# Optimization experiments

Hardware: AMD Instinct MI355X
Metric: run time of the kernel (lower is better)

The kernel has to match this reference:

```python
import jax, jax.numpy as jnp
import numpy as np

D_MODEL = 1040
N_HEADS = 16
FEAT = 32            # feature_dim
HEAD_DIM = 65        # d_model // num_heads; must equal 2*FEAT+1 for the z-division to broadcast
EPS = 1e-9


def setup_inputs() -> dict:
    key = jax.random.key(0)
    k1, k2, k3, k4, k5, k6 = jax.random.split(key, 6)
    B, S = 4, 4096
    scale = 1.0 / np.sqrt(D_MODEL)
    return {
        "hidden_states": jax.random.normal(k1, (B, S, D_MODEL), dtype=jnp.float32),
        "attention_mask": jax.random.randint(k2, (B, S), 0, 2, dtype=jnp.int32),
        "Wq": jax.random.normal(k3, (D_MODEL, N_HEADS * FEAT), dtype=jnp.float32) * scale,
        "Wk": jax.random.normal(k4, (D_MODEL, N_HEADS * FEAT), dtype=jnp.float32) * scale,
        "Wv": jax.random.normal(k5, (D_MODEL, N_HEADS * HEAD_DIM), dtype=jnp.float32) * scale,
        "Wo": jax.random.normal(k6, (N_HEADS * HEAD_DIM, D_MODEL), dtype=jnp.float32) * scale,
    }


def _phi(x):
    # polynomial feature map: [1, x, 0.5*x^2] -> last dim 2*FEAT+1
    return jnp.concatenate([jnp.ones_like(x[..., :1]), x, 0.5 * x * x], axis=-1)


def reference(hidden_states, attention_mask, Wq, Wk, Wv, Wo):
    B, S, _ = hidden_states.shape
    # projections -> [B, H, S, d]
    q = (hidden_states @ Wq).reshape(B, S, N_HEADS, FEAT).transpose(0, 2, 1, 3)
    k = (hidden_states @ Wk).reshape(B, S, N_HEADS, FEAT).transpose(0, 2, 1, 3)
    v = (hidden_states @ Wv).reshape(B, S, N_HEADS, HEAD_DIM).transpose(0, 2, 1, 3)
    q = _phi(q)  # [B, H, S, D] with D = 2*FEAT+1
    k = _phi(k)
    # linear attention: KV state then query it
    kv = jnp.einsum('bhnd,bhne->bhde', k, v)        # [B, H, D, HEAD_DIM]
    qkv = jnp.einsum('bhnd,bhde->bhne', q, kv)      # [B, H, S, HEAD_DIM]
    # z = einsum('bhnd,bhne->bhne', q, k.sum(n, keepdim)) with size-1 broadcast on n:
    # contracts d of q against k.sum's d-slot, i.e. (sum_d q) outer (sum_n k)
    z = jnp.sum(q, axis=-1, keepdims=True) * jnp.sum(k, axis=2, keepdims=True)  # [B,H,S,D]
    out = qkv / (z + EPS)                            # requires HEAD_DIM == D
    out = jnp.where(attention_mask[:, None, :, None] == 0, 0.0, out)
    out = out.transpose(0, 2, 1, 3).reshape(B, S, N_HEADS * HEAD_DIM)
    return out @ Wo
```

## Files before the change

kernel.cpp:

```cpp
#include <hip/hip_runtime.h>
#include <hip/hip_bf16.h>

typedef unsigned short ushort_t;
typedef unsigned int uint_t;

#define S_LEN 4096
#define BATCH 4
#define DMODEL 1040
#define KPAD 1056
#define KO 1152
#define NPADW 1152
#define M_H 8192
#define KVSPLIT 32

using f32x4 = __attribute__((ext_vector_type(4))) float;
using bf16x8 = __attribute__((ext_vector_type(8))) __bf16;
using f16x8 = __attribute__((ext_vector_type(8))) _Float16;

__device__ __forceinline__ void splitf16(float x, ushort_t& h, ushort_t& l) {
  _Float16 hf = (_Float16)x;
  float r = (x - (float)hf) * 4096.0f;
  _Float16 lf = (_Float16)r;
  h = __builtin_bit_cast(ushort_t, hf);
  l = __builtin_bit_cast(ushort_t, lf);
}

typedef const __attribute__((address_space(1))) unsigned int* gas_u32p;
typedef __attribute__((address_space(3))) unsigned int* las_u32p;
__device__ __forceinline__ void gload_lds16(const ushort_t* g, ushort_t* l) {
  __builtin_amdgcn_global_load_lds((gas_u32p)g, (las_u32p)l, 16, 0, 0);
}

__device__ __forceinline__ void tile_map(int lid, int NT, int& m0, int& n0) {
  const int x = lid & 7, pos = lid >> 3;
  const int mi = pos / NT, ni = pos - mi * NT;
  m0 = (x * 8 + mi) * 128;
  n0 = ni * 128;
}

union pack8 { ushort_t u[8]; uint4 v; };

__global__ __launch_bounds__(256) void split_hs_kernel(const float* __restrict__ hs,
                                                       ushort_t* __restrict__ hh,
                                                       ushort_t* __restrict__ hl) {
  const int C8 = KPAD / 8;
  int idx = blockIdx.x * 256 + threadIdx.x;
  if (idx >= M_H * C8) return;
  int row = idx / C8, col = (idx % C8) * 8;
  pack8 ph, pl;
  if (col < DMODEL) {
    const float* p = &hs[(size_t)row * DMODEL + col];
#pragma unroll
    for (int j = 0; j < 8; ++j) splitf16(p[j], ph.u[j], pl.u[j]);
  } else {
#pragma unroll
    for (int j = 0; j < 8; ++j) { ph.u[j] = 0; pl.u[j] = 0; }
  }
  size_t o = (size_t)row * KPAD + col;
  *reinterpret_cast<uint4*>(&hh[o]) = ph.v;
  *reinterpret_cast<uint4*>(&hl[o]) = pl.v;
}

__global__ __launch_bounds__(256) void split_wqk_kernel(const float* __restrict__ Wq,
                                                        const float* __restrict__ Wk,
                                                        ushort_t* __restrict__ th,
                                                        ushort_t* __restrict__ tl) {
  const int C8 = KPAD / 8;
  int idx = blockIdx.x * 256 + threadIdx.x;
  if (idx >= 1024 * C8) return;
  int n = idx / C8, k = (idx % C8) * 8;
  pack8 ph, pl;
#pragma unroll
  for (int j = 0; j < 8; ++j) {
    int kk = k + j;
    float val = 0.f;
    if (kk < DMODEL) val = (n < 512) ? Wq[(size_t)kk * 512 + n] : Wk[(size_t)kk * 512 + (n - 512)];
    splitf16(val, ph.u[j], pl.u[j]);
  }
  size_t o = (size_t)n * KPAD + k;
  *reinterpret_cast<uint4*>(&th[o]) = ph.v;
  *reinterpret_cast<uint4*>(&tl[o]) = pl.v;
}

__global__ __launch_bounds__(256) void split_wv_kernel(const float* __restrict__ Wv,
                                                       ushort_t* __restrict__ th) {
  const int C8 = KPAD / 8;
  int idx = blockIdx.x * 256 + threadIdx.x;
  if (idx >= NPADW * C8) return;
  int n = idx / C8, k = (idx % C8) * 8;
  pack8 ph;
#pragma unroll
  for (int j = 0; j < 8; ++j) {
    int kk = k + j;
    float val = (n < DMODEL && kk < DMODEL) ? Wv[(size_t)kk * DMODEL + n] : 0.f;
    ph.u[j] = __builtin_bit_cast(ushort_t, (_Float16)val);
  }
  *reinterpret_cast<uint4*>(&th[(size_t)n * KPAD + k]) = ph.v;
}

__global__ __launch_bounds__(256) void split_wo_kernel(const float* __restrict__ Wo,
                                                       ushort_t* __restrict__ th) {
  const int C8O = KO / 8;
  int idx = blockIdx.x * 256 + threadIdx.x;
  if (idx >= NPADW * C8O) return;
  int n = idx / C8O, k = (idx % C8O) * 8;
  pack8 ph;
#pragma unroll
  for (int j = 0; j < 8; ++j) {
    int kk = k + j;
    int h = kk / 72, e = kk % 72;
    float val = (n < DMODEL && e < 65) ? Wo[(size_t)(h * 65 + e) * DMODEL + n] : 0.f;
    ph.u[j] = __builtin_bit_cast(ushort_t, __float2bfloat16(val));
  }
  *reinterpret_cast<uint4*>(&th[(size_t)n * KO + k]) = ph.v;
}

__global__ __launch_bounds__(512, 4) void gemm_qk(const ushort_t* __restrict__ Ahg,
                                                  const ushort_t* __restrict__ Alg,
                                                  const ushort_t* __restrict__ Bhg,
                                                  const ushort_t* __restrict__ Blg,
                                                  float* __restrict__ C, int kdim) {
  __shared__ ushort_t Ah[2][4096], Al[2][4096], Bh[2][4096], Bl[2][4096];
  const int t = threadIdx.x;
  const int w = t >> 6, l = t & 63;
  int m0, n0;
  tile_map(blockIdx.x, 8, m0, n0);
  const int wm = w >> 2, wn = w & 3;
  const int row16 = l & 15, g = l >> 4;

  f32x4 acc[4][2], acc2[4][2];
#pragma unroll
  for (int m = 0; m < 4; ++m)
#pragma unroll
    for (int n = 0; n < 2; ++n) { acc[m][n] = (f32x4){0,0,0,0}; acc2[m][n] = (f32x4){0,0,0,0}; }

  const int chunk = t;
  const int r0 = chunk >> 2;
  const int ch0 = (chunk & 3) ^ ((r0 ^ (r0 >> 2)) & 3);

#define STAGE_QK(K0, BUF)                                                       \
  {                                                                             \
    const size_t ga = (size_t)(m0 + r0) * kdim + (K0) + ch0 * 8;                \
    const size_t gb = (size_t)(n0 + r0) * kdim + (K0) + ch0 * 8;                \
    gload_lds16(Ahg + ga, &Ah[BUF][chunk * 8]);                                 \
    gload_lds16(Alg + ga, &Al[BUF][chunk * 8]);                                 \
    gload_lds16(Bhg + gb, &Bh[BUF][chunk * 8]);                                 \
    gload_lds16(Blg + gb, &Bl[BUF][chunk * 8]);                                 \
  }

  STAGE_QK(0, 0);
  __syncthreads();
  for (int k0 = 0, it = 0; k0 < kdim; k0 += 32, ++it) {
    const int cur = it & 1;
    if (k0 + 32 < kdim) STAGE_QK(k0 + 32, cur ^ 1);
    f16x8 fah[4], fal[4], fbh[2], fbl[2];
#pragma unroll
    for (int f = 0; f < 4; ++f) {
      const int ra = wm * 64 + f * 16 + row16;
      const int ca = (g ^ ((ra ^ (ra >> 2)) & 3)) << 3;
      fah[f] = *(const f16x8*)&Ah[cur][ra * 32 + ca];
      fal[f] = *(const f16x8*)&Al[cur][ra * 32 + ca];
    }
#pragma unroll
    for (int f = 0; f < 2; ++f) {
      const int rb = wn * 32 + f * 16 + row16;
      const int cb = (g ^ ((rb ^ (rb >> 2)) & 3)) << 3;
      fbh[f] = *(const f16x8*)&Bh[cur][rb * 32 + cb];
      fbl[f] = *(const f16x8*)&Bl[cur][rb * 32 + cb];
    }
#pragma unroll
    for (int m = 0; m < 4; ++m)
#pragma unroll
      for (int n = 0; n < 2; ++n) {
        acc[m][n]  = __builtin_amdgcn_mfma_f32_16x16x32_f16(fah[m], fbh[n], acc[m][n], 0, 0, 0);
        acc2[m][n] = __builtin_amdgcn_mfma_f32_16x16x32_f16(fah[m], fbl[n], acc2[m][n], 0, 0, 0);
        acc2[m][n] = __builtin_amdgcn_mfma_f32_16x16x32_f16(fal[m], fbh[n], acc2[m][n], 0, 0, 0);
      }
    __syncthreads();
  }
#undef STAGE_QK

  const float S2 = 1.0f / 4096.0f;
#pragma unroll
  for (int m = 0; m < 4; ++m)
#pragma unroll
    for (int n = 0; n < 2; ++n) {
      const int col = n0 + wn * 32 + n * 16 + row16;
      const int rowb = m0 + wm * 64 + m * 16 + g * 4;
#pragma unroll
      for (int i = 0; i < 4; ++i)
        C[(size_t)(rowb + i) * 1024 + col] = acc[m][n][i] + acc2[m][n][i] * S2;
    }
}

__global__ __launch_bounds__(256, 4) void gemm_v(const ushort_t* __restrict__ Ahg,
                                                 const ushort_t* __restrict__ Bhg,
                                                 ushort_t* __restrict__ Cv, int kdim) {
  __shared__ ushort_t Ah[2][4096], Bh[2][4096];
  const int t = threadIdx.x;
  const int w = t >> 6, l = t & 63;
  int m0, n0;
  tile_map(blockIdx.x, 9, m0, n0);
  const int wm = w >> 1, wn = w & 1;
  const int row16 = l & 15, g = l >> 4;

  f32x4 acc[4][4];
#pragma unroll
  for (int m = 0; m < 4; ++m)
#pragma unroll
    for (int n = 0; n < 4; ++n) acc[m][n] = (f32x4){0,0,0,0};

  const int chunk0 = (w * 2 + 0) * 64 + l;
  const int chunk1 = (w * 2 + 1) * 64 + l;
  const int r0 = chunk0 >> 2, r1 = chunk1 >> 2;
  const int ch0 = (chunk0 & 3) ^ ((r0 ^ (r0 >> 2)) & 3);
  const int ch1 = (chunk1 & 3) ^ ((r1 ^ (r1 >> 2)) & 3);

#define STAGE_V(K0, BUF)                                                        \
  {                                                                             \
    const size_t ga0 = (size_t)(m0 + r0) * kdim + (K0) + ch0 * 8;               \
    const size_t gb0 = (size_t)(n0 + r0) * kdim + (K0) + ch0 * 8;               \
    const size_t ga1 = (size_t)(m0 + r1) * kdim + (K0) + ch1 * 8;               \
    const size_t gb1 = (size_t)(n0 + r1) * kdim + (K0) + ch1 * 8;               \
    gload_lds16(Ahg + ga0, &Ah[BUF][chunk0 * 8]);                               \
    gload_lds16(Bhg + gb0, &Bh[BUF][chunk0 * 8]);                               \
    gload_lds16(Ahg + ga1, &Ah[BUF][chunk1 * 8]);                               \
    gload_lds16(Bhg + gb1, &Bh[BUF][chunk1 * 8]);                               \
  }

  STAGE_V(0, 0);
  __syncthreads();
  for (int k0 = 0, it = 0; k0 < kdim; k0 += 32, ++it) {
    const int cur = it & 1;
    if (k0 + 32 < kdim) STAGE_V(k0 + 32, cur ^ 1);
    f16x8 fah[4], fbh[4];
#pragma unroll
    for (int f = 0; f < 4; ++f) {
      const int ra = wm * 64 + f * 16 + row16;
      const int ca = (g ^ ((ra ^ (ra >> 2)) & 3)) << 3;
      fah[f] = *(const f16x8*)&Ah[cur][ra * 32 + ca];
      const int rb = wn * 64 + f * 16 + row16;
      const int cb = (g ^ ((rb ^ (rb >> 2)) & 3)) << 3;
      fbh[f] = *(const f16x8*)&Bh[cur][rb * 32 + cb];
    }
#pragma unroll
    for (int m = 0; m < 4; ++m)
#pragma unroll
      for (int n = 0; n < 4; ++n)
        acc[m][n] = __builtin_amdgcn_mfma_f32_16x16x32_f16(fah[m], fbh[n], acc[m][n], 0, 0, 0);
    __syncthreads();
  }
#undef STAGE_V

#pragma unroll
  for (int m = 0; m < 4; ++m)
#pragma unroll
    for (int n = 0; n < 4; ++n) {
      const int col = n0 + wn * 64 + n * 16 + row16;
      const int rowb = m0 + wm * 64 + m * 16 + g * 4;
#pragma unroll
      for (int i = 0; i < 4; ++i)
        Cv[(size_t)(rowb + i) * 1152 + col] =
            __builtin_bit_cast(ushort_t, (_Float16)acc[m][n][i]);
    }
}

__global__ __launch_bounds__(256, 4) void gemm_o(const ushort_t* __restrict__ Ahg,
                                                 const ushort_t* __restrict__ Bhg,
                                                 float* __restrict__ C, int kdim) {
  __shared__ ushort_t Ah[2][4096], Bh[2][4096];
  const int t = threadIdx.x;
  const int w = t >> 6, l = t & 63;
  int m0, n0;
  tile_map(blockIdx.x, 9, m0, n0);
  const int wm = w >> 1, wn = w & 1;
  const int row16 = l & 15, g = l >> 4;

  f32x4 acc[4][4];
#pragma unroll
  for (int m = 0; m < 4; ++m)
#pragma unroll
    for (int n = 0; n < 4; ++n) acc[m][n] = (f32x4){0,0,0,0};

  const int chunk0 = (w * 2 + 0) * 64 + l;
  const int chunk1 = (w * 2 + 1) * 64 + l;
  const int r0 = chunk0 >> 2, r1 = chunk1 >> 2;
  const int ch0 = (chunk0 & 3) ^ ((r0 ^ (r0 >> 2)) & 3);
  const int ch1 = (chunk1 & 3) ^ ((r1 ^ (r1 >> 2)) & 3);

#define STAGE_O(K0, BUF)                                                        \
  {                                                                             \
    const size_t ga0 = (size_t)(m0 + r0) * kdim + (K0) + ch0 * 8;               \
    const size_t gb0 = (size_t)(n0 + r0) * kdim + (K0) + ch0 * 8;               \
    const size_t ga1 = (size_t)(m0 + r1) * kdim + (K0) + ch1 * 8;               \
    const size_t gb1 = (size_t)(n0 + r1) * kdim + (K0) + ch1 * 8;               \
    gload_lds16(Ahg + ga0, &Ah[BUF][chunk0 * 8]);                               \
    gload_lds16(Bhg + gb0, &Bh[BUF][chunk0 * 8]);                               \
    gload_lds16(Ahg + ga1, &Ah[BUF][chunk1 * 8]);                               \
    gload_lds16(Bhg + gb1, &Bh[BUF][chunk1 * 8]);                               \
  }

  STAGE_O(0, 0);
  __syncthreads();
  for (int k0 = 0, it = 0; k0 < kdim; k0 += 32, ++it) {
    const int cur = it & 1;
    if (k0 + 32 < kdim) STAGE_O(k0 + 32, cur ^ 1);
    bf16x8 fah[4], fbh[4];
#pragma unroll
    for (int f = 0; f < 4; ++f) {
      const int ra = wm * 64 + f * 16 + row16;
      const int ca = (g ^ ((ra ^ (ra >> 2)) & 3)) << 3;
      fah[f] = *(const bf16x8*)&Ah[cur][ra * 32 + ca];
      const int rb = wn * 64 + f * 16 + row16;
      const int cb = (g ^ ((rb ^ (rb >> 2)) & 3)) << 3;
      fbh[f] = *(const bf16x8*)&Bh[cur][rb * 32 + cb];
    }
#pragma unroll
    for (int m = 0; m < 4; ++m)
#pragma unroll
      for (int n = 0; n < 4; ++n)
        acc[m][n] = __builtin_amdgcn_mfma_f32_16x16x32_bf16(fah[m], fbh[n], acc[m][n], 0, 0, 0);
    __syncthreads();
  }
#undef STAGE_O

#pragma unroll
  for (int m = 0; m < 4; ++m)
#pragma unroll
    for (int n = 0; n < 4; ++n) {
      const int col = n0 + wn * 64 + n * 16 + row16;
      if (col < DMODEL) {
        const int rowb = m0 + wm * 64 + m * 16 + g * 4;
#pragma unroll
        for (int i = 0; i < 4; ++i) C[(size_t)(rowb + i) * DMODEL + col] = acc[m][n][i];
      }
    }
}

__global__ __launch_bounds__(256) void kv_kernel(const float* __restrict__ qk,
                                                 const ushort_t* __restrict__ vbuf,
                                                 float* __restrict__ kvpart,
                                                 float* __restrict__ kspart) {
  const int bh = blockIdx.x;
  const int split = blockIdx.y;
  const int bl = bh >> 4, h = bh & 15;
  __shared__ float ks[64][68];
  __shared__ float vs[64][68];
  const int tid = threadIdx.x;
  const int t1 = 256 + tid;
  const int d00 = (tid / 17) * 4, e00 = (tid % 17) * 4;
  const int d10 = (t1 / 17) * 4, e10 = (t1 % 17) * 4;
  float acc0[16] = {};
  float acc1[16] = {};
  float kcol = 0.f;

  for (int chunk = 0; chunk < 2; ++chunk) {
    const int nb = split * 128 + chunk * 64;
    for (int idx = tid; idx < 64 * 65; idx += 256) {
      const int r = idx / 65, d = idx % 65;
      const size_t row = (size_t)(bl * S_LEN + nb + r);
      float val;
      if (d == 0) val = 1.f;
      else if (d <= 32) val = qk[row * 1024 + 512 + h * 32 + (d - 1)];
      else {
        float x = qk[row * 1024 + 512 + h * 32 + (d - 33)];
        val = 0.5f * x * x;
      }
      ks[r][d] = val;
      vs[r][d] = (float)__builtin_bit_cast(_Float16, vbuf[row * 1152 + h * 65 + d]);
    }
    __syncthreads();
    for (int r = 0; r < 64; ++r) {
      float a[4], v[4];
#pragma unroll
      for (int i = 0; i < 4; ++i) a[i] = ks[r][d00 + i];
#pragma unroll
      for (int j = 0; j < 4; ++j) v[j] = vs[r][e00 + j];
#pragma unroll
      for (int i = 0; i < 4; ++i)
#pragma unroll
        for (int j = 0; j < 4; ++j) acc0[i * 4 + j] += a[i] * v[j];
    }
    if (tid < 33) {
      for (int r = 0; r < 64; ++r) {
        float a[4], v[4];
#pragma unroll
        for (int i = 0; i < 4; ++i) a[i] = ks[r][d10 + i];
#pragma unroll
        for (int j = 0; j < 4; ++j) v[j] = vs[r][e10 + j];
#pragma unroll
        for (int i = 0; i < 4; ++i)
#pragma unroll
          for (int j = 0; j < 4; ++j) acc1[i * 4 + j] += a[i] * v[j];
      }
    }
    if (tid < 65) {
      float s = 0.f;
      for (int r = 0; r < 64; ++r) s += ks[r][tid];
      kcol += s;
    }
    __syncthreads();
  }

  float* kvp = kvpart + ((size_t)split * 32 + bh) * 4225;
#pragma unroll
  for (int i = 0; i < 4; ++i)
#pragma unroll
    for (int j = 0; j < 4; ++j) {
      int d = d00 + i, e = e00 + j;
      if (d < 65 && e < 65) kvp[d * 65 + e] = acc0[i * 4 + j];
    }
  if (tid < 33) {
#pragma unroll
    for (int i = 0; i < 4; ++i)
#pragma unroll
      for (int j = 0; j < 4; ++j) {
        int d = d10 + i, e = e10 + j;
        if (d < 65 && e < 65) kvp[d * 65 + e] = acc1[i * 4 + j];
      }
  }
  if (tid < 65) kspart[((size_t)split * 32 + bh) * 65 + tid] = kcol;
}

__global__ __launch_bounds__(256) void kv_reduce(const float* __restrict__ kvpart,
                                                 const float* __restrict__ kspart,
                                                 float* __restrict__ kv,
                                                 float* __restrict__ ksum) {
  const int NKV = 32 * 4225;
  const int NKS = 32 * 65;
  int i = blockIdx.x * 256 + threadIdx.x;
  if (i < NKV) {
    float s = 0.f;
#pragma unroll 8
    for (int p = 0; p < KVSPLIT; ++p) s += kvpart[(size_t)p * NKV + i];
    kv[i] = s;
  } else if (i < NKV + NKS) {
    int j = i - NKV;
    float s = 0.f;
#pragma unroll 8
    for (int p = 0; p < KVSPLIT; ++p) s += kspart[p * NKS + j];
    ksum[j] = s;
  }
}

__global__ __launch_bounds__(256, 4) void qkv_kernel(const float* __restrict__ qk,
                                                     const float* __restrict__ kv,
                                                     const float* __restrict__ ksum,
                                                     const int* __restrict__ mask,
                                                     uint_t* __restrict__ ath32,
                                                     int half) {
  const int gx = blockIdx.x;
  const int bh = blockIdx.y;
  const int bl = bh >> 4, h = bh & 15;
  __shared__ float kvs[65 * 68];
  __shared__ float phis[32][68];
  __shared__ float kss[65];
  __shared__ float qsums[32];
  const int tid = threadIdx.x;

  const float* kvp = kv + (size_t)bh * 4225;
  for (int i = tid; i < 4225; i += 256) kvs[(i / 65) * 68 + (i % 65)] = kvp[i];
  for (int idx = tid; idx < 1024; idx += 256) {
    int tt = idx >> 5, f = idx & 31;
    size_t row = (size_t)(bl * S_LEN + gx * 32 + tt);
    float val = qk[row * 1024 + h * 32 + f];
    phis[tt][1 + f] = val;
    phis[tt][33 + f] = 0.5f * val * val;
  }
  if (tid < 32) phis[tid][0] = 1.f;
  if (tid < 65) kss[tid] = ksum[bh * 65 + tid];
  __syncthreads();
  if (tid < 32) {
    float s = 0.f;
    for (int d = 0; d < 65; ++d) s += phis[tid][d];
    qsums[tid] = s;
  }
  __syncthreads();

  const int tt = tid >> 3, fg = tid & 7;
  float accs[8] = {0.f, 0.f, 0.f, 0.f, 0.f, 0.f, 0.f, 0.f};
  const float* ph = phis[tt];
#pragma unroll 4
  for (int d = 0; d < 65; ++d) {
    float p = ph[d];
    const float* kr = &kvs[d * 68 + fg * 8];
    float4 va = *reinterpret_cast<const float4*>(kr);
    float4 vb = *reinterpret_cast<const float4*>(kr + 4);
    accs[0] += p * va.x; accs[1] += p * va.y; accs[2] += p * va.z; accs[3] += p * va.w;
    accs[4] += p * vb.x; accs[5] += p * vb.y; accs[6] += p * vb.z; accs[7] += p * vb.w;
  }
  float a64 = 0.f;
  if (fg == 0) {
#pragma unroll 4
    for (int d = 0; d < 65; ++d) a64 += ph[d] * kvs[d * 68 + 64];
  }

  const int s_in_b = gx * 32 + tt;
  const size_t row = (size_t)(bl * S_LEN + s_in_b);
  const int m = mask[(half * 2 + bl) * S_LEN + s_in_b];
  const float qs = qsums[tt];
  const float fm = (m == 0) ? 0.f : 1.f;
  float o[8];
#pragma unroll
  for (int j = 0; j < 8; ++j) {
    float z = qs * kss[fg * 8 + j] + 1e-9f;
    o[j] = fm * accs[j] / z;
  }
  const size_t base = row * 576 + h * 36 + fg * 4;
  pack8 phh;
#pragma unroll
  for (int j = 0; j < 8; ++j)
    phh.u[j] = __builtin_bit_cast(ushort_t, __float2bfloat16(o[j]));
  *reinterpret_cast<uint4*>(&ath32[base]) = phh.v;
  if (fg == 0) {
    float z = qs * kss[64] + 1e-9f;
    float o64 = fm * a64 / z;
    uint4 tailh = {(uint_t)__builtin_bit_cast(ushort_t, __float2bfloat16(o64)), 0u, 0u, 0u};
    *reinterpret_cast<uint4*>(&ath32[row * 576 + h * 36 + 32]) = tailh;
  }
}

extern "C" void kernel_launch(void* const* d_in, const int* in_sizes, int n_in,
                              void* d_out, int out_size, void* d_ws, size_t ws_size,
                              hipStream_t stream) {
  const float* hs = (const float*)d_in[0];
  const int* mask = (const int*)d_in[1];
  const float* Wq = (const float*)d_in[2];
  const float* Wk = (const float*)d_in[3];
  const float* Wv = (const float*)d_in[4];
  const float* Wo = (const float*)d_in[5];
  float* out = (float*)d_out;

  const size_t PLANE_HS = (size_t)M_H * KPAD;

  char* base = (char*)d_ws;
  ushort_t* hsh = (ushort_t*)base;
  ushort_t* hsl = hsh + PLANE_HS;
  uint_t* ath32 = (uint_t*)base;
  char* b1 = base + 2 * PLANE_HS * 2;
  float* qkbuf = (float*)b1;
  char* b2 = b1 + (size_t)M_H * 1024 * 4;
  ushort_t* vbuf = (ushort_t*)b2;
  char* b3 = b2 + (size_t)M_H * 1152 * 2;
  float* kv = (float*)b3;
  float* ksum = kv + 32 * 4225;
  float* kvpart = ksum + 32 * 65;
  float* kspart = kvpart + (size_t)KVSPLIT * 32 * 4225;
  char* b4 = b3 + ((size_t)(32 * 4225 + 32 * 65) * (KVSPLIT + 1)) * 4;
  ushort_t* Wqkh = (ushort_t*)b4;
  ushort_t* Wqkl = Wqkh + (size_t)1024 * KPAD;
  ushort_t* Wvh = Wqkl + (size_t)1024 * KPAD;
  ushort_t* Woh = Wvh + (size_t)NPADW * KPAD;

  dim3 blk(256);
  const int C8 = KPAD / 8;
  const int C8O = KO / 8;

  split_wqk_kernel<<<(1024 * C8 + 255) / 256, blk, 0, stream>>>(Wq, Wk, Wqkh, Wqkl);
  split_wv_kernel<<<(NPADW * C8 + 255) / 256, blk, 0, stream>>>(Wv, Wvh);
  split_wo_kernel<<<(NPADW * C8O + 255) / 256, blk, 0, stream>>>(Wo, Woh);

  for (int half = 0; half < 2; ++half) {
    const float* hs_h = hs + (size_t)half * M_H * DMODEL;
    float* out_h = out + (size_t)half * M_H * DMODEL;

    split_hs_kernel<<<(M_H * C8 + 255) / 256, blk, 0, stream>>>(hs_h, hsh, hsl);

    gemm_qk<<<512, dim3(512), 0, stream>>>(hsh, hsl, Wqkh, Wqkl, qkbuf, KPAD);
    gemm_v<<<576, blk, 0, stream>>>(hsh, Wvh, vbuf, KPAD);

    kv_kernel<<<dim3(32, KVSPLIT), blk, 0, stream>>>(qkbuf, vbuf, kvpart, kspart);
    kv_reduce<<<dim3((32 * 4225 + 32 * 65 + 255) / 256), blk, 0, stream>>>(kvpart, kspart, kv, ksum);

    qkv_kernel<<<dim3(128, 32), blk, 0, stream>>>(qkbuf, kv, ksum, mask, ath32, half);

    gemm_o<<<576, blk, 0, stream>>>((ushort_t*)ath32, Woh, out_h, KO);
  }
}
```

Before: 482.6 us.

## Use 512-thread blocks for V/O GEMMs and shrink kv_kernel LDS chunks

gemm_v and gemm_o now launch 512 threads (8 waves in a 2x4 layout) per 128x128 tile, so each wave computes a 64x32 subtile with half the accumulators, and each thread issues one staging load per matrix instead of two. kv_kernel processes four 32-row chunks instead of two 64-row chunks, halving its shared memory, and its launch bound asks for 8 blocks per CU. qkv_kernel's launch bound is raised to 6 blocks per CU. The aim is more resident waves to hide latency, at the cost of more A-fragment LDS reads per wave, more barriers in kv_kernel, and possible register spills under the tighter bounds.

```diff
diff --git a/kernel.cpp b/kernel.cpp
--- a/kernel.cpp
+++ b/kernel.cpp
@@ -193,7 +193,7 @@
     }
 }
 
-__global__ __launch_bounds__(256, 4) void gemm_v(const ushort_t* __restrict__ Ahg,
+__global__ __launch_bounds__(512, 4) void gemm_v(const ushort_t* __restrict__ Ahg,
                                                  const ushort_t* __restrict__ Bhg,
                                                  ushort_t* __restrict__ Cv, int kdim) {
   __shared__ ushort_t Ah[2][4096], Bh[2][4096];
@@ -201,31 +201,25 @@
   const int w = t >> 6, l = t & 63;
   int m0, n0;
   tile_map(blockIdx.x, 9, m0, n0);
-  const int wm = w >> 1, wn = w & 1;
+  const int wm = w >> 2, wn = w & 3;
   const int row16 = l & 15, g = l >> 4;
 
-  f32x4 acc[4][4];
+  f32x4 acc[4][2];
 #pragma unroll
   for (int m = 0; m < 4; ++m)
 #pragma unroll
-    for (int n = 0; n < 4; ++n) acc[m][n] = (f32x4){0,0,0,0};
-
-  const int chunk0 = (w * 2 + 0) * 64 + l;
-  const int chunk1 = (w * 2 + 1) * 64 + l;
-  const int r0 = chunk0 >> 2, r1 = chunk1 >> 2;
-  const int ch0 = (chunk0 & 3) ^ ((r0 ^ (r0 >> 2)) & 3);
-  const int ch1 = (chunk1 & 3) ^ ((r1 ^ (r1 >> 2)) & 3);
+    for (int n = 0; n < 2; ++n) acc[m][n] = (f32x4){0,0,0,0};
+
+  const int chunk = t;
+  const int r0 = chunk >> 2;
+  const int ch0 = (chunk & 3) ^ ((r0 ^ (r0 >> 2)) & 3);
 
 #define STAGE_V(K0, BUF)                                                        \
   {                                                                             \
-    const size_t ga0 = (size_t)(m0 + r0) * kdim + (K0) + ch0 * 8;               \
-    const size_t gb0 = (size_t)(n0 + r0) * kdim + (K0) + ch0 * 8;               \
-    const size_t ga1 = (size_t)(m0 + r1) * kdim + (K0) + ch1 * 8;               \
-    const size_t gb1 = (size_t)(n0 + r1) * kdim + (K0) + ch1 * 8;               \
-    gload_lds16(Ahg + ga0, &Ah[BUF][chunk0 * 8]);                               \
-    gload_lds16(Bhg + gb0, &Bh[BUF][chunk0 * 8]);                               \
-    gload_lds16(Ahg + ga1, &Ah[BUF][chunk1 * 8]);                               \
-    gload_lds16(Bhg + gb1, &Bh[BUF][chunk1 * 8]);                               \
+    const size_t ga = (size_t)(m0 + r0) * kdim + (K0) + ch0 * 8;                \
+    const size_t gb = (size_t)(n0 + r0) * kdim + (K0) + ch0 * 8;                \
+    gload_lds16(Ahg + ga, &Ah[BUF][chunk * 8]);                                 \
+    gload_lds16(Bhg + gb, &Bh[BUF][chunk * 8]);                                 \
   }
 
   STAGE_V(0, 0);
@@ -233,20 +227,23 @@
   for (int k0 = 0, it = 0; k0 < kdim; k0 += 32, ++it) {
     const int cur = it & 1;
     if (k0 + 32 < kdim) STAGE_V(k0 + 32, cur ^ 1);
-    f16x8 fah[4], fbh[4];
+    f16x8 fah[4], fbh[2];
 #pragma unroll
     for (int f = 0; f < 4; ++f) {
       const int ra = wm * 64 + f * 16 + row16;
       const int ca = (g ^ ((ra ^ (ra >> 2)) & 3)) << 3;
       fah[f] = *(const f16x8*)&Ah[cur][ra * 32 + ca];
-      const int rb = wn * 64 + f * 16 + row16;
+    }
+#pragma unroll
+    for (int f = 0; f < 2; ++f) {
+      const int rb = wn * 32 + f * 16 + row16;
       const int cb = (g ^ ((rb ^ (rb >> 2)) & 3)) << 3;
       fbh[f] = *(const f16x8*)&Bh[cur][rb * 32 + cb];
     }
 #pragma unroll
     for (int m = 0; m < 4; ++m)
 #pragma unroll
-      for (int n = 0; n < 4; ++n)
+      for (int n = 0; n < 2; ++n)
         acc[m][n] = __builtin_amdgcn_mfma_f32_16x16x32_f16(fah[m], fbh[n], acc[m][n], 0, 0, 0);
     __syncthreads();
   }
@@ -255,8 +252,8 @@
 #pragma unroll
   for (int m = 0; m < 4; ++m)
 #pragma unroll
-    for (int n = 0; n < 4; ++n) {
-      const int col = n0 + wn * 64 + n * 16 + row16;
+    for (int n = 0; n < 2; ++n) {
+      const int col = n0 + wn * 32 + n * 16 + row16;
       const int rowb = m0 + wm * 64 + m * 16 + g * 4;
 #pragma unroll
       for (int i = 0; i < 4; ++i)
@@ -265,7 +262,7 @@
     }
 }
 
-__global__ __launch_bounds__(256, 4) void gemm_o(const ushort_t* __restrict__ Ahg,
+__global__ __launch_bounds__(512, 4) void gemm_o(const ushort_t* __restrict__ Ahg,
                                                  const ushort_t* __restrict__ Bhg,
                                                  float* __restrict__ C, int kdim) {
   __shared__ ushort_t Ah[2][4096], Bh[2][4096];
@@ -273,31 +270,25 @@
   const int w = t >> 6, l = t & 63;
   int m0, n0;
   tile_map(blockIdx.x, 9, m0, n0);
-  const int wm = w >> 1, wn = w & 1;
+  const int wm = w >> 2, wn = w & 3;
   const int row16 = l & 15, g = l >> 4;
 
-  f32x4 acc[4][4];
+  f32x4 acc[4][2];
 #pragma unroll
   for (int m = 0; m < 4; ++m)
 #pragma unroll
-    for (int n = 0; n < 4; ++n) acc[m][n] = (f32x4){0,0,0,0};
-
-  const int chunk0 = (w * 2 + 0) * 64 + l;
-  const int chunk1 = (w * 2 + 1) * 64 + l;
-  const int r0 = chunk0 >> 2, r1 = chunk1 >> 2;
-  const int ch0 = (chunk0 & 3) ^ ((r0 ^ (r0 >> 2)) & 3);
-  const int ch1 = (chunk1 & 3) ^ ((r1 ^ (r1 >> 2)) & 3);
+    for (int n = 0; n < 2; ++n) acc[m][n] = (f32x4){0,0,0,0};
+
+  const int chunk = t;
+  const int r0 = chunk >> 2;
+  const int ch0 = (chunk & 3) ^ ((r0 ^ (r0 >> 2)) & 3);
 
 #define STAGE_O(K0, BUF)                                                        \
   {                                                                             \
-    const size_t ga0 = (size_t)(m0 + r0) * kdim + (K0) + ch0 * 8;               \
-    const size_t gb0 = (size_t)(n0 + r0) * kdim + (K0) + ch0 * 8;               \
-    const size_t ga1 = (size_t)(m0 + r1) * kdim + (K0) + ch1 * 8;               \
-    const size_t gb1 = (size_t)(n0 + r1) * kdim + (K0) + ch1 * 8;               \
-    gload_lds16(Ahg + ga0, &Ah[BUF][chunk0 * 8]);                               \
-    gload_lds16(Bhg + gb0, &Bh[BUF][chunk0 * 8]);                               \
-    gload_lds16(Ahg + ga1, &Ah[BUF][chunk1 * 8]);                               \
-    gload_lds16(Bhg + gb1, &Bh[BUF][chunk1 * 8]);                               \
+    const size_t ga = (size_t)(m0 + r0) * kdim + (K0) + ch0 * 8;                \
+    const size_t gb = (size_t)(n0 + r0) * kdim + (K0) + ch0 * 8;                \
+    gload_lds16(Ahg + ga, &Ah[BUF][chunk * 8]);                                 \
+    gload_lds16(Bhg + gb, &Bh[BUF][chunk * 8]);                                 \
   }
 
   STAGE_O(0, 0);
@@ -305,20 +296,23 @@
   for (int k0 = 0, it = 0; k0 < kdim; k0 += 32, ++it) {
     const int cur = it & 1;
     if (k0 + 32 < kdim) STAGE_O(k0 + 32, cur ^ 1);
-    bf16x8 fah[4], fbh[4];
+    bf16x8 fah[4], fbh[2];
 #pragma unroll
     for (int f = 0; f < 4; ++f) {
       const int ra = wm * 64 + f * 16 + row16;
       const int ca = (g ^ ((ra ^ (ra >> 2)) & 3)) << 3;
       fah[f] = *(const bf16x8*)&Ah[cur][ra * 32 + ca];
-      const int rb = wn * 64 + f * 16 + row16;
+    }
+#pragma unroll
+    for (int f = 0; f < 2; ++f) {
+      const int rb = wn * 32 + f * 16 + row16;
       const int cb = (g ^ ((rb ^ (rb >> 2)) & 3)) << 3;
       fbh[f] = *(const bf16x8*)&Bh[cur][rb * 32 + cb];
     }
 #pragma unroll
     for (int m = 0; m < 4; ++m)
 #pragma unroll
-      for (int n = 0; n < 4; ++n)
+      for (int n = 0; n < 2; ++n)
         acc[m][n] = __builtin_amdgcn_mfma_f32_16x16x32_bf16(fah[m], fbh[n], acc[m][n], 0, 0, 0);
     __syncthreads();
   }
@@ -327,8 +321,8 @@
 #pragma unroll
   for (int m = 0; m < 4; ++m)
 #pragma unroll
-    for (int n = 0; n < 4; ++n) {
-      const int col = n0 + wn * 64 + n * 16 + row16;
+    for (int n = 0; n < 2; ++n) {
+      const int col = n0 + wn * 32 + n * 16 + row16;
       if (col < DMODEL) {
         const int rowb = m0 + wm * 64 + m * 16 + g * 4;
 #pragma unroll
@@ -337,15 +331,15 @@
     }
 }
 
-__global__ __launch_bounds__(256) void kv_kernel(const float* __restrict__ qk,
-                                                 const ushort_t* __restrict__ vbuf,
-                                                 float* __restrict__ kvpart,
-                                                 float* __restrict__ kspart) {
+__global__ __launch_bounds__(256, 8) void kv_kernel(const float* __restrict__ qk,
+                                                    const ushort_t* __restrict__ vbuf,
+                                                    float* __restrict__ kvpart,
+                                                    float* __restrict__ kspart) {
   const int bh = blockIdx.x;
   const int split = blockIdx.y;
   const int bl = bh >> 4, h = bh & 15;
-  __shared__ float ks[64][68];
-  __shared__ float vs[64][68];
+  __shared__ float ks[32][68];
+  __shared__ float vs[32][68];
   const int tid = threadIdx.x;
   const int t1 = 256 + tid;
   const int d00 = (tid / 17) * 4, e00 = (tid % 17) * 4;
@@ -354,9 +348,9 @@
   float acc1[16] = {};
   float kcol = 0.f;
 
-  for (int chunk = 0; chunk < 2; ++chunk) {
-    const int nb = split * 128 + chunk * 64;
-    for (int idx = tid; idx < 64 * 65; idx += 256) {
+  for (int chunk = 0; chunk < 4; ++chunk) {
+    const int nb = split * 128 + chunk * 32;
+    for (int idx = tid; idx < 32 * 65; idx += 256) {
       const int r = idx / 65, d = idx % 65;
       const size_t row = (size_t)(bl * S_LEN + nb + r);
       float val;
@@ -370,7 +364,7 @@
       vs[r][d] = (float)__builtin_bit_cast(_Float16, vbuf[row * 1152 + h * 65 + d]);
     }
     __syncthreads();
-    for (int r = 0; r < 64; ++r) {
+    for (int r = 0; r < 32; ++r) {
       float a[4], v[4];
 #pragma unroll
       for (int i = 0; i < 4; ++i) a[i] = ks[r][d00 + i];
@@ -382,7 +376,7 @@
         for (int j = 0; j < 4; ++j) acc0[i * 4 + j] += a[i] * v[j];
     }
     if (tid < 33) {
-      for (int r = 0; r < 64; ++r) {
+      for (int r = 0; r < 32; ++r) {
         float a[4], v[4];
 #pragma unroll
         for (int i = 0; i < 4; ++i) a[i] = ks[r][d10 + i];
@@ -396,7 +390,7 @@
     }
     if (tid < 65) {
       float s = 0.f;
-      for (int r = 0; r < 64; ++r) s += ks[r][tid];
+      for (int r = 0; r < 32; ++r) s += ks[r][tid];
       kcol += s;
     }
     __syncthreads();
@@ -443,7 +437,7 @@
   }
 }
 
-__global__ __launch_bounds__(256, 4) void qkv_kernel(const float* __restrict__ qk,
+__global__ __launch_bounds__(256, 6) void qkv_kernel(const float* __restrict__ qk,
                                                      const float* __restrict__ kv,
                                                      const float* __restrict__ ksum,
                                                      const int* __restrict__ mask,
@@ -567,13 +561,13 @@
     split_hs_kernel<<<(M_H * C8 + 255) / 256, blk, 0, stream>>>(hs_h, hsh, hsl);
 
     gemm_qk<<<512, dim3(512), 0, stream>>>(hsh, hsl, Wqkh, Wqkl, qkbuf, KPAD);
-    gemm_v<<<576, blk, 0, stream>>>(hsh, Wvh, vbuf, KPAD);
+    gemm_v<<<576, dim3(512), 0, stream>>>(hsh, Wvh, vbuf, KPAD);
 
     kv_kernel<<<dim3(32, KVSPLIT), blk, 0, stream>>>(qkbuf, vbuf, kvpart, kspart);
     kv_reduce<<<dim3((32 * 4225 + 32 * 65 + 255) / 256), blk, 0, stream>>>(kvpart, kspart, kv, ksum);
 
     qkv_kernel<<<dim3(128, 32), blk, 0, stream>>>(qkbuf, kv, ksum, mask, ath32, half);
 
-    gemm_o<<<576, blk, 0, stream>>>((ushort_t*)ath32, Woh, out_h, KO);
-  }
-}
+    gemm_o<<<576, dim3(512), 0, stream>>>((ushort_t*)ath32, Woh, out_h, KO);
+  }
+}
```

Result: slower. 1.422 ms (+194.7%).
